# Kernel optimization log

Measured on AMD Instinct MI355X. Metric: run time of the kernel, lower is better.

## Reference

```python
import jax, jax.numpy as jnp
import numpy as np

LN_EPS = 1e-5
DIM = 8        # pooled spatial size per axis -> token feature = DIM*DIM = 64
DIM_HEAD = 64


def setup_inputs() -> dict:
    key = jax.random.key(0)
    k1, k2, k3 = jax.random.split(key, 3)
    b, t, c, h, w = 8, 16, 64, 56, 56
    x = jax.random.normal(k1, (b, t, c, h, w), dtype=jnp.float32)
    pos_embedding = jax.random.normal(k2, (b * c, t, DIM * DIM), dtype=jnp.float32)
    # nn.Linear(dim*dim, 2*dim_head, bias=False); stored here as (in, out)
    W_qk = jax.random.normal(k3, (DIM * DIM, 2 * DIM_HEAD), dtype=jnp.float32) * (DIM * DIM) ** -0.5
    gamma = jnp.ones((DIM * DIM,), dtype=jnp.float32)
    beta = jnp.zeros((DIM * DIM,), dtype=jnp.float32)
    return {"x": x, "pos_embedding": pos_embedding, "W_qk": W_qk, "gamma": gamma, "beta": beta}


def reference(x, pos_embedding, W_qk, gamma, beta):
    b, t, c, h, w = x.shape
    scale = DIM_HEAD ** -0.5
    # AdaptiveAvgPool3d((None, DIM, DIM)): h,w divisible by DIM -> exact mean pool
    ph, pw = h // DIM, w // DIM
    pooled = x.reshape(b, t, c, DIM, ph, DIM, pw).mean(axis=(4, 6))  # (b,t,c,DIM,DIM)
    # rearrange 'b t c h w -> (b c) t (h w)'
    s = jnp.transpose(pooled, (0, 2, 1, 3, 4)).reshape(b * c, t, DIM * DIM)
    s = s + pos_embedding
    # LayerNorm over last dim
    mu = s.mean(axis=-1, keepdims=True)
    var = s.var(axis=-1, keepdims=True)
    s = (s - mu) * jax.lax.rsqrt(var + LN_EPS) * gamma + beta
    qk = s @ W_qk                                   # (bc, t, 2*dim_head)
    q, k = jnp.split(qk, 2, axis=-1)
    v = jnp.transpose(x, (0, 2, 1, 3, 4)).reshape(b * c, t, h * w)
    dots = jnp.einsum('bid,bjd->bij', q, k) * scale  # (bc, t, t)
    attn = jax.nn.softmax(dots, axis=-1)             # dropout in eval mode = identity
    out = jnp.einsum('bij,bjf->bif', attn, v)        # (bc, t, h*w)
    out = out.reshape(b, c, t, h, w).transpose(0, 2, 1, 3, 4)
    return out + x
```

## Files before the change

kernel.cpp:

```cpp
#include <hip/hip_runtime.h>
#include <hip/hip_bf16.h>
#include <math.h>


#define HW 3136
#define HW4 784
#define TSTRIDE4 50176

__global__ __launch_bounds__(256) void pool_kernel(const float* __restrict__ x,
                                                   const float* __restrict__ pos,
                                                   float* __restrict__ s_ws) {
    __shared__ float plane[HW];
    const int p   = blockIdx.x;
    const int tid = threadIdx.x;

    const float4* xp = reinterpret_cast<const float4*>(x + (size_t)p * HW);
    float4* pl4 = reinterpret_cast<float4*>(plane);
    #pragma unroll
    for (int k = 0; k < 3; k++) pl4[tid + k * 256] = xp[tid + k * 256];
    if (tid < 16) pl4[768 + tid] = xp[768 + tid];
    __syncthreads();

    if (tid < 64) {
        const int i = tid >> 3, j = tid & 7;
        const float* base = plane + (i * 7) * 56 + j * 7;
        float sum = 0.f;
        #pragma unroll
        for (int r = 0; r < 7; r++) {
            #pragma unroll
            for (int cc = 0; cc < 7; cc++) sum += base[r * 56 + cc];
        }
        const int c = p & 63, t = (p >> 6) & 15, b = p >> 10;
        const int bc = b * 64 + c;
        const int off = ((bc << 4) + t) * 64 + tid;
        s_ws[off] = sum * (1.0f / 49.0f) + pos[off];
    }
}

__global__ __launch_bounds__(64) void attn_kernel(const float* __restrict__ s_ws,
                                                  const float* __restrict__ W,
                                                  const float* __restrict__ gamma,
                                                  const float* __restrict__ beta,
                                                  float* __restrict__ attn_ws) {
    __shared__ float s_lds[16 * 64];
    __shared__ float q_lds[16 * 65];
    __shared__ float k_lds[16 * 65];
    __shared__ float d_lds[256];

    const int bc   = blockIdx.x;
    const int lane = threadIdx.x;

    float wq[64], wk[64];
    #pragma unroll
    for (int d = 0; d < 64; d++) {
        wq[d] = W[d * 128 + lane];
        wk[d] = W[d * 128 + 64 + lane];
    }

    const float4* S4 = reinterpret_cast<const float4*>(s_ws + (size_t)bc * 1024);
    float4* s4 = reinterpret_cast<float4*>(s_lds);
    #pragma unroll
    for (int k = 0; k < 4; k++) s4[lane + k * 64] = S4[lane + k * 64];
    const float g   = gamma[lane];
    const float bta = beta[lane];
    __syncthreads();

    for (int r = 0; r < 16; r++) {
        float v = s_lds[r * 64 + lane];
        float sum = v, sq = v * v;
        #pragma unroll
        for (int off = 32; off > 0; off >>= 1) {
            sum += __shfl_xor(sum, off, 64);
            sq  += __shfl_xor(sq,  off, 64);
        }
        const float mu  = sum * (1.0f / 64.0f);
        const float var = sq * (1.0f / 64.0f) - mu * mu;
        s_lds[r * 64 + lane] = (v - mu) * rsqrtf(var + 1e-5f) * g + bta;
    }
    __syncthreads();

    for (int r = 0; r < 16; r++) {
        float q = 0.f, kk = 0.f;
        #pragma unroll
        for (int dd = 0; dd < 16; dd++) {
            const float4 sv = *reinterpret_cast<const float4*>(&s_lds[r * 64 + dd * 4]);
            q  += sv.x * wq[dd * 4 + 0] + sv.y * wq[dd * 4 + 1]
                + sv.z * wq[dd * 4 + 2] + sv.w * wq[dd * 4 + 3];
            kk += sv.x * wk[dd * 4 + 0] + sv.y * wk[dd * 4 + 1]
                + sv.z * wk[dd * 4 + 2] + sv.w * wk[dd * 4 + 3];
        }
        q_lds[r * 65 + lane] = q;
        k_lds[r * 65 + lane] = kk;
    }
    __syncthreads();

    const int i = lane >> 2, j0 = lane & 3;
    #pragma unroll
    for (int jj = 0; jj < 4; jj++) {
        const int j = jj * 4 + j0;
        float acc = 0.f;
        #pragma unroll
        for (int d = 0; d < 64; d++)
            acc += q_lds[i * 65 + d] * k_lds[j * 65 + d];
        d_lds[i * 16 + j] = acc * 0.125f;
    }
    __syncthreads();

    if (lane < 16) {
        float m = -1e30f;
        #pragma unroll
        for (int j = 0; j < 16; j++) m = fmaxf(m, d_lds[lane * 16 + j]);
        float e[16];
        float ssum = 0.f;
        #pragma unroll
        for (int j = 0; j < 16; j++) { e[j] = __expf(d_lds[lane * 16 + j] - m); ssum += e[j]; }
        const float inv = 1.0f / ssum;
        #pragma unroll
        for (int j = 0; j < 16; j++)
            d_lds[lane * 16 + j] = e[j] * inv + (j == lane ? 1.0f : 0.0f);
    }
    __syncthreads();

    #pragma unroll
    for (int k = 0; k < 4; k++)
        attn_ws[bc * 256 + k * 64 + lane] = d_lds[k * 64 + lane];
}

__device__ __forceinline__ void acc4(float4& a, float w, const float4& v) {
    a.x += w * v.x; a.y += w * v.y; a.z += w * v.z; a.w += w * v.w;
}

__global__ __launch_bounds__(256) void apply_kernel(const float* __restrict__ x,
                                                    const float* __restrict__ attn_ws,
                                                    float* __restrict__ out) {
    const int bc   = blockIdx.x;
    const int half = blockIdx.y;
    const int tid  = threadIdx.x;
    const int b = bc >> 6, c = bc & 63;

    const float4* x4 = reinterpret_cast<const float4*>(x);
    float4* o4 = reinterpret_cast<float4*>(out);
    const float4* A4 = reinterpret_cast<const float4*>(attn_ws + (size_t)bc * 256);
    const size_t plane0 = ((size_t)b * 1024 + c) * HW4;

    #pragma unroll
    for (int k = 0; k < 2; k++) {
        const int rem = 392 - k * 256;
        if (tid < rem) {
            const size_t f4 = (size_t)half * 392 + k * 256 + tid;
            float4 xv[16];
            #pragma unroll
            for (int j = 0; j < 16; j++)
                xv[j] = x4[plane0 + (size_t)j * TSTRIDE4 + f4];
            #pragma unroll
            for (int t = 0; t < 16; t++) {
                float4 a; a.x = 0.f; a.y = 0.f; a.z = 0.f; a.w = 0.f;
                #pragma unroll
                for (int jj = 0; jj < 4; jj++) {
                    const float4 w4 = A4[t * 4 + jj];
                    acc4(a, w4.x, xv[jj * 4 + 0]);
                    acc4(a, w4.y, xv[jj * 4 + 1]);
                    acc4(a, w4.z, xv[jj * 4 + 2]);
                    acc4(a, w4.w, xv[jj * 4 + 3]);
                }
                o4[plane0 + (size_t)t * TSTRIDE4 + f4] = a;
            }
        }
    }
}

extern "C" void kernel_launch(void* const* d_in, const int* in_sizes, int n_in,
                              void* d_out, int out_size, void* d_ws, size_t ws_size,
                              hipStream_t stream) {
    (void)in_sizes; (void)n_in; (void)out_size; (void)ws_size;
    const float* x     = (const float*)d_in[0];
    const float* pos   = (const float*)d_in[1];
    const float* W     = (const float*)d_in[2];
    const float* gamma = (const float*)d_in[3];
    const float* beta  = (const float*)d_in[4];
    float* out = (float*)d_out;

    float* s_ws    = (float*)d_ws;
    float* attn_ws = s_ws + 512 * 16 * 64;

    pool_kernel<<<8192, 256, 0, stream>>>(x, pos, s_ws);
    attn_kernel<<<512, 64, 0, stream>>>(s_ws, W, gamma, beta, attn_ws);
    apply_kernel<<<dim3(512, 2), 256, 0, stream>>>(x, attn_ws, out);
}
```

Before: 70.55 us.

## Fuse attention computation into apply kernel and prefetch x during attention

Merges the attention (LayerNorm, QK projection, softmax) kernel into the apply kernel, so each block computes its 16x16 attention matrix in LDS and applies it directly. The first x tile is loaded into registers before the attention math, overlapping that global load latency with the computation. The work is also redistributed across 256 threads instead of 64. This removes a kernel launch and the attention workspace round trip, but halves the grid to 512 blocks with a serial loop over the plane, which may reduce parallelism and raise register pressure.

```diff
diff --git a/kernel.cpp b/kernel.cpp
--- a/kernel.cpp
+++ b/kernel.cpp
@@ -37,134 +37,131 @@
     }
 }
 
-__global__ __launch_bounds__(64) void attn_kernel(const float* __restrict__ s_ws,
-                                                  const float* __restrict__ W,
-                                                  const float* __restrict__ gamma,
-                                                  const float* __restrict__ beta,
-                                                  float* __restrict__ attn_ws) {
+__device__ __forceinline__ void acc4(float4& a, float w, const float4& v) {
+    a.x += w * v.x; a.y += w * v.y; a.z += w * v.z; a.w += w * v.w;
+}
+
+__global__ __launch_bounds__(256) void attn_apply_kernel(const float* __restrict__ x,
+                                                         const float* __restrict__ s_ws,
+                                                         const float* __restrict__ W,
+                                                         const float* __restrict__ gamma,
+                                                         const float* __restrict__ beta,
+                                                         float* __restrict__ out) {
     __shared__ float s_lds[16 * 64];
     __shared__ float q_lds[16 * 65];
     __shared__ float k_lds[16 * 65];
-    __shared__ float d_lds[256];
+    __shared__ float A[256];
 
-    const int bc   = blockIdx.x;
-    const int lane = threadIdx.x;
+    const int bc  = blockIdx.x;
+    const int tid = threadIdx.x;
+    const int b = bc >> 6, c = bc & 63;
 
-    float wq[64], wk[64];
+    const float4* x4 = reinterpret_cast<const float4*>(x);
+    float4* o4 = reinterpret_cast<float4*>(out);
+    const size_t plane0 = ((size_t)b * 1024 + c) * HW4;
+
+    float4 xv[16];
     #pragma unroll
-    for (int d = 0; d < 64; d++) {
-        wq[d] = W[d * 128 + lane];
-        wk[d] = W[d * 128 + 64 + lane];
-    }
+    for (int j = 0; j < 16; j++)
+        xv[j] = x4[plane0 + (size_t)j * TSTRIDE4 + tid];
 
     const float4* S4 = reinterpret_cast<const float4*>(s_ws + (size_t)bc * 1024);
-    float4* s4 = reinterpret_cast<float4*>(s_lds);
-    #pragma unroll
-    for (int k = 0; k < 4; k++) s4[lane + k * 64] = S4[lane + k * 64];
-    const float g   = gamma[lane];
-    const float bta = beta[lane];
+    reinterpret_cast<float4*>(s_lds)[tid] = S4[tid];
     __syncthreads();
 
-    for (int r = 0; r < 16; r++) {
-        float v = s_lds[r * 64 + lane];
-        float sum = v, sq = v * v;
+    {
+        const int row = tid >> 4, sub = tid & 15;
+        float4 v = *reinterpret_cast<const float4*>(&s_lds[row * 64 + sub * 4]);
+        float sum = v.x + v.y + v.z + v.w;
+        float sq  = v.x * v.x + v.y * v.y + v.z * v.z + v.w * v.w;
         #pragma unroll
-        for (int off = 32; off > 0; off >>= 1) {
+        for (int off = 8; off > 0; off >>= 1) {
             sum += __shfl_xor(sum, off, 64);
             sq  += __shfl_xor(sq,  off, 64);
         }
         const float mu  = sum * (1.0f / 64.0f);
         const float var = sq * (1.0f / 64.0f) - mu * mu;
-        s_lds[r * 64 + lane] = (v - mu) * rsqrtf(var + 1e-5f) * g + bta;
+        const float rs  = rsqrtf(var + 1e-5f);
+        const float4 g  = *reinterpret_cast<const float4*>(&gamma[sub * 4]);
+        const float4 bt = *reinterpret_cast<const float4*>(&beta[sub * 4]);
+        float4 o;
+        o.x = (v.x - mu) * rs * g.x + bt.x;
+        o.y = (v.y - mu) * rs * g.y + bt.y;
+        o.z = (v.z - mu) * rs * g.z + bt.z;
+        o.w = (v.w - mu) * rs * g.w + bt.w;
+        *reinterpret_cast<float4*>(&s_lds[row * 64 + sub * 4]) = o;
     }
     __syncthreads();
 
-    for (int r = 0; r < 16; r++) {
-        float q = 0.f, kk = 0.f;
+    {
+        const int col = tid & 127;
+        const int rb  = (tid >> 7) * 8;
+        float wcol[64];
         #pragma unroll
-        for (int dd = 0; dd < 16; dd++) {
-            const float4 sv = *reinterpret_cast<const float4*>(&s_lds[r * 64 + dd * 4]);
-            q  += sv.x * wq[dd * 4 + 0] + sv.y * wq[dd * 4 + 1]
-                + sv.z * wq[dd * 4 + 2] + sv.w * wq[dd * 4 + 3];
-            kk += sv.x * wk[dd * 4 + 0] + sv.y * wk[dd * 4 + 1]
-                + sv.z * wk[dd * 4 + 2] + sv.w * wk[dd * 4 + 3];
+        for (int d = 0; d < 64; d++) wcol[d] = W[d * 128 + col];
+        float qa[8];
+        #pragma unroll
+        for (int r = 0; r < 8; r++) {
+            float a = 0.f;
+            #pragma unroll
+            for (int dd = 0; dd < 16; dd++) {
+                const float4 sv = *reinterpret_cast<const float4*>(&s_lds[(rb + r) * 64 + dd * 4]);
+                a += sv.x * wcol[dd * 4 + 0] + sv.y * wcol[dd * 4 + 1]
+                   + sv.z * wcol[dd * 4 + 2] + sv.w * wcol[dd * 4 + 3];
+            }
+            qa[r] = a;
         }
-        q_lds[r * 65 + lane] = q;
-        k_lds[r * 65 + lane] = kk;
+        if (col < 64) {
+            #pragma unroll
+            for (int r = 0; r < 8; r++) q_lds[(rb + r) * 65 + col] = qa[r];
+        } else {
+            #pragma unroll
+            for (int r = 0; r < 8; r++) k_lds[(rb + r) * 65 + (col - 64)] = qa[r];
+        }
     }
     __syncthreads();
 
-    const int i = lane >> 2, j0 = lane & 3;
-    #pragma unroll
-    for (int jj = 0; jj < 4; jj++) {
-        const int j = jj * 4 + j0;
-        float acc = 0.f;
+    {
+        const int i = tid >> 4, j = tid & 15;
+        float dot = 0.f;
         #pragma unroll
         for (int d = 0; d < 64; d++)
-            acc += q_lds[i * 65 + d] * k_lds[j * 65 + d];
-        d_lds[i * 16 + j] = acc * 0.125f;
+            dot += q_lds[i * 65 + d] * k_lds[j * 65 + d];
+        dot *= 0.125f;
+        float m = dot;
+        #pragma unroll
+        for (int off = 8; off > 0; off >>= 1)
+            m = fmaxf(m, __shfl_xor(m, off, 64));
+        const float e = __expf(dot - m);
+        float es = e;
+        #pragma unroll
+        for (int off = 8; off > 0; off >>= 1)
+            es += __shfl_xor(es, off, 64);
+        A[i * 16 + j] = e / es + (i == j ? 1.0f : 0.0f);
     }
     __syncthreads();
 
-    if (lane < 16) {
-        float m = -1e30f;
-        #pragma unroll
-        for (int j = 0; j < 16; j++) m = fmaxf(m, d_lds[lane * 16 + j]);
-        float e[16];
-        float ssum = 0.f;
-        #pragma unroll
-        for (int j = 0; j < 16; j++) { e[j] = __expf(d_lds[lane * 16 + j] - m); ssum += e[j]; }
-        const float inv = 1.0f / ssum;
-        #pragma unroll
-        for (int j = 0; j < 16; j++)
-            d_lds[lane * 16 + j] = e[j] * inv + (j == lane ? 1.0f : 0.0f);
-    }
-    __syncthreads();
-
-    #pragma unroll
-    for (int k = 0; k < 4; k++)
-        attn_ws[bc * 256 + k * 64 + lane] = d_lds[k * 64 + lane];
-}
-
-__device__ __forceinline__ void acc4(float4& a, float w, const float4& v) {
-    a.x += w * v.x; a.y += w * v.y; a.z += w * v.z; a.w += w * v.w;
-}
-
-__global__ __launch_bounds__(256) void apply_kernel(const float* __restrict__ x,
-                                                    const float* __restrict__ attn_ws,
-                                                    float* __restrict__ out) {
-    const int bc   = blockIdx.x;
-    const int half = blockIdx.y;
-    const int tid  = threadIdx.x;
-    const int b = bc >> 6, c = bc & 63;
-
-    const float4* x4 = reinterpret_cast<const float4*>(x);
-    float4* o4 = reinterpret_cast<float4*>(out);
-    const float4* A4 = reinterpret_cast<const float4*>(attn_ws + (size_t)bc * 256);
-    const size_t plane0 = ((size_t)b * 1024 + c) * HW4;
-
-    #pragma unroll
-    for (int k = 0; k < 2; k++) {
-        const int rem = 392 - k * 256;
-        if (tid < rem) {
-            const size_t f4 = (size_t)half * 392 + k * 256 + tid;
-            float4 xv[16];
+    #pragma unroll 1
+    for (int k = 0; k < 4; k++) {
+        const int f4i = tid + k * 256;
+        if (k > 0) {
+            if (f4i >= HW4) break;
             #pragma unroll
             for (int j = 0; j < 16; j++)
-                xv[j] = x4[plane0 + (size_t)j * TSTRIDE4 + f4];
+                xv[j] = x4[plane0 + (size_t)j * TSTRIDE4 + f4i];
+        }
+        #pragma unroll
+        for (int t = 0; t < 16; t++) {
+            float4 a; a.x = 0.f; a.y = 0.f; a.z = 0.f; a.w = 0.f;
             #pragma unroll
-            for (int t = 0; t < 16; t++) {
-                float4 a; a.x = 0.f; a.y = 0.f; a.z = 0.f; a.w = 0.f;
-                #pragma unroll
-                for (int jj = 0; jj < 4; jj++) {
-                    const float4 w4 = A4[t * 4 + jj];
-                    acc4(a, w4.x, xv[jj * 4 + 0]);
-                    acc4(a, w4.y, xv[jj * 4 + 1]);
-                    acc4(a, w4.z, xv[jj * 4 + 2]);
-                    acc4(a, w4.w, xv[jj * 4 + 3]);
-                }
-                o4[plane0 + (size_t)t * TSTRIDE4 + f4] = a;
+            for (int jj = 0; jj < 4; jj++) {
+                const float4 w4 = *reinterpret_cast<const float4*>(&A[t * 16 + jj * 4]);
+                acc4(a, w4.x, xv[jj * 4 + 0]);
+                acc4(a, w4.y, xv[jj * 4 + 1]);
+                acc4(a, w4.z, xv[jj * 4 + 2]);
+                acc4(a, w4.w, xv[jj * 4 + 3]);
             }
+            o4[plane0 + (size_t)t * TSTRIDE4 + f4i] = a;
         }
     }
 }
@@ -180,10 +177,8 @@
     const float* beta  = (const float*)d_in[4];
     float* out = (float*)d_out;
 
-    float* s_ws    = (float*)d_ws;
-    float* attn_ws = s_ws + 512 * 16 * 64;
+    float* s_ws = (float*)d_ws;
 
     pool_kernel<<<8192, 256, 0, stream>>>(x, pos, s_ws);
-    attn_kernel<<<512, 64, 0, stream>>>(s_ws, W, gamma, beta, attn_ws);
-    apply_kernel<<<dim3(512, 2), 256, 0, stream>>>(x, attn_ws, out);
+    attn_apply_kernel<<<512, 256, 0, stream>>>(x, s_ws, W, gamma, beta, out);
 }
```

Measured after the change: 118.0 us. 67.2% more time.
